# Kernel optimization log

Hardware: AMD Instinct MI355X
Metric: run time of the kernel (lower is better)

## Reference

```python
import jax, jax.numpy as jnp
import numpy as np
import math

B, C_IN, C_OUT, K, H = 4, 128, 128, 3, 16
A = C_IN // 8  # attn_dim = in_channels // 8 per 'individual' mode


def setup_inputs() -> dict:
    key = jax.random.key(0)
    ks = jax.random.split(key, 8)
    s = 0.02
    return {
        "x": jax.random.normal(ks[0], (B, C_IN, H, H), jnp.float32),
        "weight": jax.random.normal(ks[1], (C_OUT, C_IN, K, K), jnp.float32) * s,
        "fc_q_w": jax.random.normal(ks[2], (A, C_IN), jnp.float32) * s,
        "fc_q_b": jnp.zeros((A,), jnp.float32),
        "fc_k_w": jax.random.normal(ks[3], (A, 1), jnp.float32) * s,
        "fc_k_b": jnp.zeros((A,), jnp.float32),
        "fc_v_w": jax.random.normal(ks[4], (A, 1), jnp.float32) * s,
        "fc_v_b": jnp.zeros((A,), jnp.float32),
        "fc_o_w": jax.random.normal(ks[5], (1, A), jnp.float32) * s,
        "fc_o_b": jnp.zeros((1,), jnp.float32),
        "gamma": jax.random.normal(ks[6], (1,), jnp.float32),
    }


def reference(x, weight, fc_q_w, fc_q_b, fc_k_w, fc_k_b, fc_v_w, fc_v_b,
              fc_o_w, fc_o_b, gamma):
    b, c_in, h, w_sp = x.shape
    c_out, _, kh, kw = weight.shape
    wflat = weight.reshape(-1)                                 # [Wn]
    xt = x.reshape(b, c_in, -1).transpose(0, 2, 1)             # [B, HW, C_in]
    # AttnOverWeight (mode='individual')
    q = xt @ fc_q_w.T + fc_q_b                                 # [B, HW, A]
    k = wflat[:, None] * fc_k_w[:, 0][None, :] + fc_k_b        # [Wn, A] (Linear(1,A))
    v = wflat[:, None] * fc_v_w[:, 0][None, :] + fc_v_b        # [Wn, A]
    scores = jnp.einsum('bqa,na->bqn', q, k) / math.sqrt(q.shape[-1])
    attn = jax.nn.softmax(scores, axis=2)                      # [B, HW, Wn]
    attn_out = attn.mean(axis=1)[:, :, None] * v[None]         # [B, Wn, A]
    weighted_w = (attn_out @ fc_o_w.T + fc_o_b)[..., 0]        # [B, Wn]
    masked_w = wflat[None, :] + gamma * weighted_w             # [B, Wn]
    # per-sample conv via grouped conv (groups = batch)
    kernels = masked_w.reshape(b * c_out, c_in, kh, kw)
    xg = x.reshape(1, b * c_in, h, w_sp)
    out = jax.lax.conv_general_dilated(
        xg, kernels, window_strides=(1, 1), padding=[(1, 1), (1, 1)],
        feature_group_count=b, dimension_numbers=('NCHW', 'OIHW', 'NCHW'))
    return out.reshape(b, c_out, out.shape[2], out.shape[3])
```

## Files before the change

### kernel.cpp

```cpp
#include <hip/hip_runtime.h>

#define B_      4
#define CIN     128
#define COUT    128
#define KSZ     3
#define HSP     16
#define HW      256
#define WN      147456
#define WPK     1152
#define ADIM    16

#define WS_G     0
#define WS_G0    128
#define WS_S1    129
#define WS_S0    130
#define WS_BO    131
#define WS_A     132
#define WS_PART  160
#define NBLK_MOM 144

__device__ __forceinline__ float waveReduceSum(float v) {
    #pragma unroll
    for (int off = 32; off; off >>= 1) v += __shfl_down(v, off, 64);
    return v;
}

__device__ __forceinline__ float blockReduceSum256(float v, float* tmp4, int tid) {
    v = waveReduceSum(v);
    __syncthreads();
    if ((tid & 63) == 0) tmp4[tid >> 6] = v;
    __syncthreads();
    return tmp4[0] + tmp4[1] + tmp4[2] + tmp4[3];
}

__global__ __launch_bounds__(256) void k_moments(
        const float* __restrict__ w,
        const float* __restrict__ fcq,  const float* __restrict__ fcqb,
        const float* __restrict__ fck,
        const float* __restrict__ fcv,  const float* __restrict__ fcvb,
        const float* __restrict__ fco,  const float* __restrict__ fcob,
        float* __restrict__ ws) {
    __shared__ float tmp4[4];
    const int tid = threadIdx.x, blk = blockIdx.x;

    const float4 w4 = *reinterpret_cast<const float4*>(w + (size_t)(blk * 256 + tid) * 4);
    float m0 = 0.f, m1 = 0.f, m2 = 0.f, m3 = 0.f, m4 = 0.f, m5 = 0.f;
    float vals[4] = {w4.x, w4.y, w4.z, w4.w};
    #pragma unroll
    for (int i = 0; i < 4; ++i) {
        float v = vals[i], v2 = v * v, v3 = v2 * v;
        m0 += v; m1 += v2; m2 += v3; m3 += v2 * v2; m4 += v2 * v3; m5 += v3 * v3;
    }
    float ms[6] = {m0, m1, m2, m3, m4, m5};
    #pragma unroll
    for (int k = 0; k < 6; ++k) {
        float s = blockReduceSum256(ms[k], tmp4, tid);
        if (tid == 0) ws[WS_PART + blk * 6 + k] = s;
    }
    if (blk == 0) {
        if (tid < 128) {
            float s = 0.f;
            #pragma unroll
            for (int a = 0; a < ADIM; ++a) s += fcq[a * CIN + tid] * fck[a];
            ws[WS_G + tid] = s;
        } else if (tid == 128) {
            float s = 0.f;
            for (int a = 0; a < ADIM; ++a) s += fcqb[a] * fck[a];
            ws[WS_G0] = s;
        } else if (tid == 129) {
            float s = 0.f;
            for (int a = 0; a < ADIM; ++a) s += fcv[a] * fco[a];
            ws[WS_S1] = s;
        } else if (tid == 130) {
            float s = 0.f;
            for (int a = 0; a < ADIM; ++a) s += fcvb[a] * fco[a];
            ws[WS_S0] = s;
        } else if (tid == 131) {
            ws[WS_BO] = fcob[0];
        }
    }
}

__global__ __launch_bounds__(256) void k_alpha(
        const float* __restrict__ x, float* __restrict__ ws) {
    __shared__ float tmp4[4];
    __shared__ float S[7];
    __shared__ float gl[128];
    __shared__ float g0s;
    const int tid = threadIdx.x, b = blockIdx.x;

    #pragma unroll
    for (int k = 0; k < 6; ++k) {
        float v = (tid < NBLK_MOM) ? ws[WS_PART + tid * 6 + k] : 0.f;
        float s = blockReduceSum256(v, tmp4, tid);
        if (tid == 0) S[k + 1] = s;
    }
    if (tid < 128) gl[tid] = ws[WS_G + tid];
    if (tid == 128) g0s = ws[WS_G0];
    __syncthreads();

    float dot = g0s;
    const float* xb = x + (size_t)b * CIN * HW + tid;
    #pragma unroll 8
    for (int c = 0; c < CIN; ++c) dot += xb[c * HW] * gl[c];
    const float alpha = dot * 0.25f;

    float Z = S[6] * (1.f / 720.f);
    Z = Z * alpha + S[5] * (1.f / 120.f);
    Z = Z * alpha + S[4] * (1.f / 24.f);
    Z = Z * alpha + S[3] * (1.f / 6.f);
    Z = Z * alpha + S[2] * 0.5f;
    Z = Z * alpha + S[1];
    Z = Z * alpha + (float)WN;

    const float r = 1.0f / ((float)HW * Z);

    float t = r;
    const float invk[7] = {1.f, 1.f, 0.5f, 1.f / 3.f, 0.25f, 0.2f, 1.f / 6.f};
    #pragma unroll
    for (int k = 0; k < 7; ++k) {
        float s = blockReduceSum256(t, tmp4, tid);
        if (tid == 0) ws[WS_A + b * 7 + k] = s;
        t = t * alpha * invk[k + 1 > 6 ? 6 : k + 1];
    }
}

#define CTILE 8
__global__ __launch_bounds__(256) void k_conv(
        const float* __restrict__ x, const float* __restrict__ w,
        const float* __restrict__ ws, const float* __restrict__ gamma,
        float* __restrict__ out) {
    __shared__ float mw[WPK];
    __shared__ float xp[CTILE][18][18];
    const int tid = threadIdx.x;
    const int blk = blockIdx.x;
    const int b = blk >> 7, co = blk & 127;

    const float A0 = ws[WS_A + b * 7 + 0], A1 = ws[WS_A + b * 7 + 1];
    const float A2 = ws[WS_A + b * 7 + 2], A3 = ws[WS_A + b * 7 + 3];
    const float A4 = ws[WS_A + b * 7 + 4], A5 = ws[WS_A + b * 7 + 5];
    const float A6 = ws[WS_A + b * 7 + 6];
    const float s1 = ws[WS_S1], s0 = ws[WS_S0], bo = ws[WS_BO];
    const float gam = gamma[0];

    for (int i = tid; i < WPK; i += 256) {
        float wv = w[(size_t)co * WPK + i];
        float p = A6;
        p = p * wv + A5; p = p * wv + A4; p = p * wv + A3;
        p = p * wv + A2; p = p * wv + A1; p = p * wv + A0;
        mw[i] = wv + gam * (p * (s1 * wv + s0) + bo);
    }
    {
        float* xpf = &xp[0][0][0];
        for (int i = tid; i < CTILE * 18 * 18; i += 256) xpf[i] = 0.f;
    }
    const int ox = tid & 15, oy = tid >> 4;
    float acc = 0.f;
    const float* xb = x + (size_t)b * CIN * HW;

    for (int c0 = 0; c0 < CIN; c0 += CTILE) {
        __syncthreads();
        #pragma unroll
        for (int cc = 0; cc < CTILE; ++cc)
            xp[cc][oy + 1][ox + 1] = xb[(c0 + cc) * HW + tid];
        __syncthreads();
        #pragma unroll
        for (int cc = 0; cc < CTILE; ++cc) {
            const float* mwp = &mw[(c0 + cc) * 9];
            #pragma unroll
            for (int ky = 0; ky < 3; ++ky)
                #pragma unroll
                for (int kx = 0; kx < 3; ++kx)
                    acc += xp[cc][oy + ky][ox + kx] * mwp[ky * 3 + kx];
        }
    }
    out[(size_t)blk * HW + tid] = acc;
}

extern "C" void kernel_launch(void* const* d_in, const int* in_sizes, int n_in,
                              void* d_out, int out_size, void* d_ws, size_t ws_size,
                              hipStream_t stream) {
    const float* x    = (const float*)d_in[0];
    const float* wt   = (const float*)d_in[1];
    const float* fcq  = (const float*)d_in[2];
    const float* fcqb = (const float*)d_in[3];
    const float* fck  = (const float*)d_in[4];
    const float* fcv  = (const float*)d_in[6];
    const float* fcvb = (const float*)d_in[7];
    const float* fco  = (const float*)d_in[8];
    const float* fcob = (const float*)d_in[9];
    const float* gam  = (const float*)d_in[10];
    float* ws  = (float*)d_ws;
    float* out = (float*)d_out;

    hipLaunchKernelGGL(k_moments, dim3(NBLK_MOM), dim3(256), 0, stream,
                       wt, fcq, fcqb, fck, fcv, fcvb, fco, fcob, ws);
    hipLaunchKernelGGL(k_alpha, dim3(B_), dim3(256), 0, stream, x, ws);
    hipLaunchKernelGGL(k_conv, dim3(B_ * COUT), dim3(256), 0, stream,
                       x, wt, ws, gam, out);
}
```

Before: 115.3 us.

## Replace scalar direct conv with bf16 MFMA implicit GEMM over pre-transposed operands

Splits the conv into a masked-weight kernel that writes per-sample bf16 weights in a [b][tap][co][ci] layout, a padded channel-last bf16 transpose of x, and an MFMA 16x16x32 bf16 implicit-GEMM conv kernel. The alpha kernel is also widened to 1024 threads, with the channel dot product split across four groups. The aim is to move the roughly 150 MFLOP conv onto matrix cores instead of scalar FMAs from LDS. In exchange it adds extra launches and global intermediates, drops the inputs to bf16 precision, and runs only 128 single-wave blocks in the conv with no LDS reuse.

```diff
diff --git a/kernel.cpp b/kernel.cpp
--- a/kernel.cpp
+++ b/kernel.cpp
@@ -3,8 +3,6 @@
 #define B_      4
 #define CIN     128
 #define COUT    128
-#define KSZ     3
-#define HSP     16
 #define HW      256
 #define WN      147456
 #define WPK     1152
@@ -18,6 +16,17 @@
 #define WS_A     132
 #define WS_PART  160
 #define NBLK_MOM 144
+#define MWT_OFF  4096
+#define XT_OFF   (4096 + 4*9*128*128*2)
+
+typedef __attribute__((ext_vector_type(8))) short bf16x8;
+typedef __attribute__((ext_vector_type(4))) float f32x4;
+
+__device__ __forceinline__ unsigned short f2bf(float f) {
+    union { float f; unsigned int u; } v; v.f = f;
+    unsigned int u = v.u;
+    return (unsigned short)((u + 0x7FFFu + ((u >> 16) & 1u)) >> 16);
+}
 
 __device__ __forceinline__ float waveReduceSum(float v) {
     #pragma unroll
@@ -25,12 +34,23 @@
     return v;
 }
 
-__device__ __forceinline__ float blockReduceSum256(float v, float* tmp4, int tid) {
+__device__ __forceinline__ float blockSum256(float v, float* tmp4, int tid) {
     v = waveReduceSum(v);
     __syncthreads();
     if ((tid & 63) == 0) tmp4[tid >> 6] = v;
     __syncthreads();
     return tmp4[0] + tmp4[1] + tmp4[2] + tmp4[3];
+}
+
+__device__ __forceinline__ float blockSum1024(float v, float* tmp16, int tid) {
+    v = waveReduceSum(v);
+    __syncthreads();
+    if ((tid & 63) == 0) tmp16[tid >> 6] = v;
+    __syncthreads();
+    float s = 0.f;
+    #pragma unroll
+    for (int i = 0; i < 16; ++i) s += tmp16[i];
+    return s;
 }
 
 __global__ __launch_bounds__(256) void k_moments(
@@ -54,7 +74,7 @@
     float ms[6] = {m0, m1, m2, m3, m4, m5};
     #pragma unroll
     for (int k = 0; k < 6; ++k) {
-        float s = blockReduceSum256(ms[k], tmp4, tid);
+        float s = blockSum256(ms[k], tmp4, tid);
         if (tid == 0) ws[WS_PART + blk * 6 + k] = s;
     }
     if (blk == 0) {
@@ -81,61 +101,60 @@
     }
 }
 
-__global__ __launch_bounds__(256) void k_alpha(
+__global__ __launch_bounds__(1024) void k_alpha(
         const float* __restrict__ x, float* __restrict__ ws) {
-    __shared__ float tmp4[4];
+    __shared__ float tmp16[16];
     __shared__ float S[7];
     __shared__ float gl[128];
     __shared__ float g0s;
+    __shared__ float psum[4][256];
     const int tid = threadIdx.x, b = blockIdx.x;
+    const int p = tid & 255, cg = tid >> 8;
 
     #pragma unroll
     for (int k = 0; k < 6; ++k) {
         float v = (tid < NBLK_MOM) ? ws[WS_PART + tid * 6 + k] : 0.f;
-        float s = blockReduceSum256(v, tmp4, tid);
+        float s = blockSum1024(v, tmp16, tid);
         if (tid == 0) S[k + 1] = s;
     }
     if (tid < 128) gl[tid] = ws[WS_G + tid];
     if (tid == 128) g0s = ws[WS_G0];
     __syncthreads();
 
-    float dot = g0s;
-    const float* xb = x + (size_t)b * CIN * HW + tid;
+    float dot = 0.f;
+    const float* xb = x + (size_t)b * CIN * HW + p;
+    const int c0 = cg * 32;
     #pragma unroll 8
-    for (int c = 0; c < CIN; ++c) dot += xb[c * HW] * gl[c];
-    const float alpha = dot * 0.25f;
-
-    float Z = S[6] * (1.f / 720.f);
-    Z = Z * alpha + S[5] * (1.f / 120.f);
-    Z = Z * alpha + S[4] * (1.f / 24.f);
-    Z = Z * alpha + S[3] * (1.f / 6.f);
-    Z = Z * alpha + S[2] * 0.5f;
-    Z = Z * alpha + S[1];
-    Z = Z * alpha + (float)WN;
-
-    const float r = 1.0f / ((float)HW * Z);
-
+    for (int c = 0; c < 32; ++c) dot += xb[(c0 + c) * HW] * gl[c0 + c];
+    psum[cg][p] = dot;
+    __syncthreads();
+
+    float alpha = 0.f, r = 0.f;
+    if (cg == 0) {
+        alpha = (psum[0][p] + psum[1][p] + psum[2][p] + psum[3][p] + g0s) * 0.25f;
+        float Z = S[6] * (1.f / 720.f);
+        Z = Z * alpha + S[5] * (1.f / 120.f);
+        Z = Z * alpha + S[4] * (1.f / 24.f);
+        Z = Z * alpha + S[3] * (1.f / 6.f);
+        Z = Z * alpha + S[2] * 0.5f;
+        Z = Z * alpha + S[1];
+        Z = Z * alpha + (float)WN;
+        r = 1.0f / ((float)HW * Z);
+    }
     float t = r;
     const float invk[7] = {1.f, 1.f, 0.5f, 1.f / 3.f, 0.25f, 0.2f, 1.f / 6.f};
     #pragma unroll
     for (int k = 0; k < 7; ++k) {
-        float s = blockReduceSum256(t, tmp4, tid);
+        float s = blockSum1024(t, tmp16, tid);
         if (tid == 0) ws[WS_A + b * 7 + k] = s;
         t = t * alpha * invk[k + 1 > 6 ? 6 : k + 1];
     }
 }
 
-#define CTILE 8
-__global__ __launch_bounds__(256) void k_conv(
-        const float* __restrict__ x, const float* __restrict__ w,
-        const float* __restrict__ ws, const float* __restrict__ gamma,
-        float* __restrict__ out) {
-    __shared__ float mw[WPK];
-    __shared__ float xp[CTILE][18][18];
-    const int tid = threadIdx.x;
-    const int blk = blockIdx.x;
-    const int b = blk >> 7, co = blk & 127;
-
+__global__ __launch_bounds__(256) void k_mask(
+        const float* __restrict__ w, const float* __restrict__ ws,
+        const float* __restrict__ gamma, unsigned short* __restrict__ mwT) {
+    const int b = blockIdx.x >> 3, chunk = blockIdx.x & 7;
     const float A0 = ws[WS_A + b * 7 + 0], A1 = ws[WS_A + b * 7 + 1];
     const float A2 = ws[WS_A + b * 7 + 2], A3 = ws[WS_A + b * 7 + 3];
     const float A4 = ws[WS_A + b * 7 + 4], A5 = ws[WS_A + b * 7 + 5];
@@ -143,38 +162,93 @@
     const float s1 = ws[WS_S1], s0 = ws[WS_S0], bo = ws[WS_BO];
     const float gam = gamma[0];
 
-    for (int i = tid; i < WPK; i += 256) {
-        float wv = w[(size_t)co * WPK + i];
-        float p = A6;
-        p = p * wv + A5; p = p * wv + A4; p = p * wv + A3;
-        p = p * wv + A2; p = p * wv + A1; p = p * wv + A0;
-        mw[i] = wv + gam * (p * (s1 * wv + s0) + bo);
-    }
-    {
-        float* xpf = &xp[0][0][0];
-        for (int i = tid; i < CTILE * 18 * 18; i += 256) xpf[i] = 0.f;
-    }
-    const int ox = tid & 15, oy = tid >> 4;
-    float acc = 0.f;
-    const float* xb = x + (size_t)b * CIN * HW;
-
-    for (int c0 = 0; c0 < CIN; c0 += CTILE) {
-        __syncthreads();
-        #pragma unroll
-        for (int cc = 0; cc < CTILE; ++cc)
-            xp[cc][oy + 1][ox + 1] = xb[(c0 + cc) * HW + tid];
-        __syncthreads();
-        #pragma unroll
-        for (int cc = 0; cc < CTILE; ++cc) {
-            const float* mwp = &mw[(c0 + cc) * 9];
+    const int end = chunk * 2048 + 2048;
+    for (int i = chunk * 2048 + threadIdx.x; i < end; i += 256) {
+        const int co = i >> 7, ci = i & 127;
+        const float* wp = w + co * WPK + ci * 9;
+        #pragma unroll
+        for (int j = 0; j < 9; ++j) {
+            float wv = wp[j];
+            float pp = A6;
+            pp = pp * wv + A5; pp = pp * wv + A4; pp = pp * wv + A3;
+            pp = pp * wv + A2; pp = pp * wv + A1; pp = pp * wv + A0;
+            float mwv = wv + gam * (pp * (s1 * wv + s0) + bo);
+            mwT[(((b * 9 + j) << 7 | co) << 7) | ci] = f2bf(mwv);
+        }
+    }
+}
+
+__global__ __launch_bounds__(256) void k_xt(
+        const float* __restrict__ x, unsigned short* __restrict__ xT) {
+    const int b = blockIdx.x, tid = threadIdx.x;
+    if (tid < 68) {
+        int rr, cc;
+        if (tid < 18)      { rr = 0;            cc = tid; }
+        else if (tid < 36) { rr = 17;           cc = tid - 18; }
+        else if (tid < 52) { rr = tid - 36 + 1; cc = 0; }
+        else               { rr = tid - 52 + 1; cc = 17; }
+        unsigned short* dst = xT + ((size_t)b * 324 + rr * 18 + cc) * 128;
+        bf16x8 z = {};
+        #pragma unroll
+        for (int i = 0; i < 16; ++i) *reinterpret_cast<bf16x8*>(dst + i * 8) = z;
+    }
+    const int py = tid >> 4, px = tid & 15;
+    const float* xb = x + (size_t)b * CIN * HW + tid;
+    unsigned short* dst = xT + ((size_t)b * 324 + (py + 1) * 18 + (px + 1)) * 128;
+    for (int ci0 = 0; ci0 < 128; ci0 += 8) {
+        bf16x8 pk;
+        #pragma unroll
+        for (int e = 0; e < 8; ++e) pk[e] = (short)f2bf(xb[(ci0 + e) * HW]);
+        *reinterpret_cast<bf16x8*>(dst + ci0) = pk;
+    }
+}
+
+__global__ __launch_bounds__(64) void k_conv_mfma(
+        const unsigned short* __restrict__ mwT,
+        const unsigned short* __restrict__ xT,
+        float* __restrict__ out) {
+    const int wgid = blockIdx.x;
+    const int l = threadIdx.x;
+    const int b = wgid >> 5;
+    const int rem = wgid & 31;
+    const int cobase = (rem >> 3) * 32;
+    const int pbase  = (rem & 7) * 32;
+    const int lr = l & 15, lk = l >> 4;
+
+    const int p0 = pbase + lr,       p1 = pbase + 16 + lr;
+    const int py0 = p0 >> 4, px0 = p0 & 15;
+    const int py1 = p1 >> 4, px1 = p1 & 15;
+
+    f32x4 acc[2][2] = {};
+
+    #pragma unroll 1
+    for (int j = 0; j < 9; ++j) {
+        const int dy = j / 3, dx = j % 3;
+        const unsigned short* ab = mwT + (((b * 9 + j) * 128 + cobase + lr) * 128 + lk * 8);
+        const unsigned short* bb0 = xT + (((size_t)b * 324 + (py0 + dy) * 18 + (px0 + dx)) * 128 + lk * 8);
+        const unsigned short* bb1 = xT + (((size_t)b * 324 + (py1 + dy) * 18 + (px1 + dx)) * 128 + lk * 8);
+        #pragma unroll
+        for (int c = 0; c < 4; ++c) {
+            bf16x8 a0 = *reinterpret_cast<const bf16x8*>(ab + c * 32);
+            bf16x8 a1 = *reinterpret_cast<const bf16x8*>(ab + 16 * 128 + c * 32);
+            bf16x8 vb0 = *reinterpret_cast<const bf16x8*>(bb0 + c * 32);
+            bf16x8 vb1 = *reinterpret_cast<const bf16x8*>(bb1 + c * 32);
+            acc[0][0] = __builtin_amdgcn_mfma_f32_16x16x32_bf16(a0, vb0, acc[0][0], 0, 0, 0);
+            acc[0][1] = __builtin_amdgcn_mfma_f32_16x16x32_bf16(a0, vb1, acc[0][1], 0, 0, 0);
+            acc[1][0] = __builtin_amdgcn_mfma_f32_16x16x32_bf16(a1, vb0, acc[1][0], 0, 0, 0);
+            acc[1][1] = __builtin_amdgcn_mfma_f32_16x16x32_bf16(a1, vb1, acc[1][1], 0, 0, 0);
+        }
+    }
+    #pragma unroll
+    for (int s = 0; s < 2; ++s)
+        #pragma unroll
+        for (int t = 0; t < 2; ++t)
             #pragma unroll
-            for (int ky = 0; ky < 3; ++ky)
-                #pragma unroll
-                for (int kx = 0; kx < 3; ++kx)
-                    acc += xp[cc][oy + ky][ox + kx] * mwp[ky * 3 + kx];
-        }
-    }
-    out[(size_t)blk * HW + tid] = acc;
+            for (int r = 0; r < 4; ++r) {
+                const int co = cobase + s * 16 + lk * 4 + r;
+                const int p  = pbase + t * 16 + lr;
+                out[((size_t)b * COUT + co) * HW + p] = acc[s][t][r];
+            }
 }
 
 extern "C" void kernel_launch(void* const* d_in, const int* in_sizes, int n_in,
@@ -191,11 +265,14 @@
     const float* fcob = (const float*)d_in[9];
     const float* gam  = (const float*)d_in[10];
     float* ws  = (float*)d_ws;
+    unsigned short* mwT = (unsigned short*)((char*)d_ws + MWT_OFF);
+    unsigned short* xT  = (unsigned short*)((char*)d_ws + XT_OFF);
     float* out = (float*)d_out;
 
     hipLaunchKernelGGL(k_moments, dim3(NBLK_MOM), dim3(256), 0, stream,
                        wt, fcq, fcqb, fck, fcv, fcvb, fco, fcob, ws);
-    hipLaunchKernelGGL(k_alpha, dim3(B_), dim3(256), 0, stream, x, ws);
-    hipLaunchKernelGGL(k_conv, dim3(B_ * COUT), dim3(256), 0, stream,
-                       x, wt, ws, gam, out);
-}
+    hipLaunchKernelGGL(k_alpha, dim3(B_), dim3(1024), 0, stream, x, ws);
+    hipLaunchKernelGGL(k_mask, dim3(32), dim3(256), 0, stream, wt, ws, gam, mwT);
+    hipLaunchKernelGGL(k_xt, dim3(B_), dim3(256), 0, stream, x, xT);
+    hipLaunchKernelGGL(k_conv_mfma, dim3(128), dim3(64), 0, stream, mwT, xT, out);
+}
```

Measured after the change: 107.4 us. 6.9% less time.
